# Kernel tuning notes

Measured on AMD Instinct MI355X. Metric: run time of the kernel, lower is better.

The kernel has to match this reference:

```python
import jax, jax.numpy as jnp
import numpy as np

P = 0.8  # DropConnect keep probability
KERNELS = (3, 2)


def eps_contract(core, x, ks):
    """Contract one EPS core with all sliding ks x ks windows of x.
    core: (out, q**(ks*ks)); x: (b, h, w, q) -> (b, h-ks+1, w-ks+1, out).
    Builds the window tensor-product incrementally (small fixed ks*ks loop)."""
    b, h, w, q = x.shape
    H, W = h - ks + 1, w - ks + 1
    prod = None
    for di in range(ks):
        for dj in range(ks):
            pix = x[:, di:di + H, dj:dj + W, :]  # (b, H, W, q)
            if prod is None:
                prod = pix
            else:
                prod = (prod[..., :, None] * pix[..., None, :]).reshape(b, H, W, -1)
    # prod: (b, H, W, q**(ks*ks))
    return jnp.einsum('bhwk,ok->bhwo', prod, core)


def dropconnect_epses(epses):
    """Bernoulli(P) mask each core's components, rescale by 1/P (training mode)."""
    mkey = jax.random.key(42)
    out = []
    for i, core in enumerate(epses):
        mask = (jax.random.uniform(jax.random.fold_in(mkey, i), core.shape) < P).astype(core.dtype)
        out.append(mask * core / P)
    return out


def setup_inputs() -> dict:
    key = jax.random.key(0)
    k0, k1, k2, k3 = jax.random.split(key, 4)
    b = 128
    x = jax.random.uniform(k0, (b, 28, 28, 2), jnp.float32)  # quantum-encoded image
    d0 = 2 ** (3 * 3)   # 512 : first core input dim (q=2, ks=3)
    d1 = 6 ** (2 * 2)   # 1296: second core input dim (q=6, ks=2)
    eps0 = jax.random.normal(k1, (6, d0), jnp.float32) * d0 ** -0.5
    eps1 = jax.random.normal(k2, (10, d1), jnp.float32) * d1 ** -0.5
    in_features = 25 * 25 * 10  # (28 - (3+2) + 2)^2 * out_q
    W = jax.random.normal(k3, (10, in_features), jnp.float32) * (in_features ** -0.5 / 4.0)
    bias = jnp.zeros((10,), jnp.float32)
    return {"x": x, "eps0": eps0, "eps1": eps1, "W": W, "bias": bias}


def reference(x, eps0, eps1, W, bias):
    e0, e1 = dropconnect_epses((eps0, eps1))
    h = eps_contract(e0, x, KERNELS[0])   # (b, 26, 26, 6)
    h = eps_contract(e1, h, KERNELS[1])   # (b, 25, 25, 10)
    flat = h.reshape(h.shape[0], -1)      # b (h w q)
    return flat @ W.T + bias
```

## Files before the change

kernel.cpp:

```cpp
#include <hip/hip_runtime.h>
#include <hip/hip_bf16.h>
#include <stdint.h>

typedef __attribute__((ext_vector_type(8))) short short8;
typedef __attribute__((ext_vector_type(4))) float floatx4;
typedef __attribute__((ext_vector_type(4))) int intx4;

__device__ float h_g[128 * 4056];

__device__ __forceinline__ void threefry2x32(uint32_t k0, uint32_t k1,
                                             uint32_t& x0, uint32_t& x1) {
  const uint32_t ks2 = k0 ^ k1 ^ 0x1BD11BDAu;
  uint32_t ks[3] = {k0, k1, ks2};
  const int rot[8] = {13, 15, 26, 6, 17, 29, 16, 24};
  x0 += ks[0];
  x1 += ks[1];
#pragma unroll
  for (int i = 0; i < 5; ++i) {
#pragma unroll
    for (int j = 0; j < 4; ++j) {
      const int r = rot[(i & 1) * 4 + j];
      x0 += x1;
      x1 = (x1 << r) | (x1 >> (32 - r));
      x1 ^= x0;
    }
    x0 += ks[(i + 1) % 3];
    x1 += ks[(i + 2) % 3] + (uint32_t)(i + 1);
  }
}

struct TFPair { uint32_t x0, x1; };
constexpr TFPair tf_const(uint32_t k0, uint32_t k1, uint32_t x0, uint32_t x1) {
  const uint32_t ks2 = k0 ^ k1 ^ 0x1BD11BDAu;
  uint32_t ks[3] = {k0, k1, ks2};
  const int rot[8] = {13, 15, 26, 6, 17, 29, 16, 24};
  x0 += ks[0];
  x1 += ks[1];
  for (int i = 0; i < 5; ++i) {
    for (int j = 0; j < 4; ++j) {
      const int r = rot[(i & 1) * 4 + j];
      x0 += x1;
      x1 = (x1 << r) | (x1 >> (32 - r));
      x1 ^= x0;
    }
    x0 += ks[(i + 1) % 3];
    x1 += ks[(i + 2) % 3] + (uint32_t)(i + 1);
  }
  return {x0, x1};
}
constexpr TFPair FOLD0 = tf_const(0u, 42u, 0u, 0u);
constexpr TFPair FOLD1 = tf_const(0u, 42u, 0u, 1u);

__device__ __forceinline__ float dropmask(int core, int e, float v) {
  const uint32_t f0 = core ? FOLD1.x0 : FOLD0.x0;
  const uint32_t f1 = core ? FOLD1.x1 : FOLD0.x1;
  uint32_t a = 0u, b = (uint32_t)e;
  threefry2x32(f0, f1, a, b);
  uint32_t bits = a ^ b;
  float u = __uint_as_float((bits >> 9) | 0x3F800000u) - 1.0f;
  float m = (u < 0.8f) ? 1.0f : 0.0f;
  return v * m / 0.8f;
}

__device__ __forceinline__ unsigned short f2bf(float f) {
  uint32_t u = __float_as_uint(f);
  uint32_t r = u + 0x7fffu + ((u >> 16) & 1u);
  return (unsigned short)(r >> 16);
}

union B2I { __hip_bfloat162 b; int i; };
__device__ __forceinline__ int pk_bf16(float lo, float hi) {
  B2I u;
  u.b = __float22bfloat162_rn(make_float2(lo, hi));
  return u.i;
}
union Frag { intx4 i; short8 s; };

__global__ void prep_kernel(const float* __restrict__ eps0,
                            const float* __restrict__ eps1,
                            unsigned short* __restrict__ bsw1,
                            unsigned short* __restrict__ bsw2,
                            const float* __restrict__ bias,
                            float* __restrict__ out) {
  int idx = blockIdx.x * 256 + threadIdx.x;
  if (idx < 1280) out[idx] = bias[idx % 10];
  if (idx < 8192) {
    int j = idx & 7, L = (idx >> 3) & 63, c = idx >> 9;
    int o = L & 15, q = L >> 4;
    int k = c * 32 + q * 8 + j;
    float v = 0.0f;
    if (o < 6) {
      int e = o * 512 + k;
      v = dropmask(0, e, eps0[e]);
    }
    bsw1[idx] = f2bf(v);
  } else {
    int t2 = idx - 8192;
    int j = t2 & 7, L = (t2 >> 3) & 63, c = t2 >> 9;
    int o = L & 15, q = L >> 4;
    int t = 45 * q + c;
    int m = t / 5, nk = 8 * (t % 5) + j;
    float v = 0.0f;
    if (o < 10 && nk < 36) {
      int e = o * 1296 + m * 36 + nk;
      v = dropmask(1, e, eps1[e]);
    }
    bsw2[t2] = f2bf(v);
  }
}

__device__ __forceinline__ float sel6(const float a[6], int k) {
  float r = a[0];
  r = (k == 1) ? a[1] : r;
  r = (k == 2) ? a[2] : r;
  r = (k == 3) ? a[3] : r;
  r = (k == 4) ? a[4] : r;
  r = (k == 5) ? a[5] : r;
  return r;
}

__global__ __launch_bounds__(256, 4) void stage1_kernel(
    const float* __restrict__ x, const unsigned short* __restrict__ bsw1) {
  const int b = blockIdx.y;
  const int t1 = blockIdx.x * 4 + (threadIdx.x >> 6);
  if (t1 >= 43) return;
  const int lane = threadIdx.x & 63;
  const int col = lane & 15, q = lane >> 4;

  intx4 bfr1[16];
  const intx4* bsrc1 = (const intx4*)bsw1;
#pragma unroll
  for (int c = 0; c < 16; ++c) bfr1[c] = bsrc1[c * 64 + lane];

  const float2* x2 = (const float2*)x + b * 784;
  const int p_raw = t1 * 16 + col;
  const int p = p_raw < 676 ? p_raw : 675;
  const int ii = p / 26, jj = p - (p / 26) * 26;

  float xv[9][2];
#pragma unroll
  for (int di = 0; di < 3; ++di)
#pragma unroll
    for (int dj = 0; dj < 3; ++dj) {
      float2 v = x2[(ii + di) * 28 + (jj + dj)];
      xv[di * 3 + dj][0] = v.x;
      xv[di * 3 + dj][1] = v.y;
    }

  float w3[8];
#pragma unroll
  for (int j = 0; j < 8; ++j)
    w3[j] = xv[6][(j >> 2) & 1] * xv[7][(j >> 1) & 1] * xv[8][j & 1];

  const float wq = xv[4][(q >> 1) & 1] * xv[5][q & 1];
  float t01[4], t23[4];
#pragma unroll
  for (int a = 0; a < 2; ++a)
#pragma unroll
    for (int d = 0; d < 2; ++d) {
      t01[a * 2 + d] = xv[0][a] * xv[1][d];
      t23[a * 2 + d] = xv[2][a] * xv[3][d] * wq;
    }

  floatx4 acc0 = {0.f, 0.f, 0.f, 0.f};
  floatx4 acc1 = {0.f, 0.f, 0.f, 0.f};
#pragma unroll
  for (int c = 0; c < 16; ++c) {
    Frag bf;
    bf.i = bfr1[c];
    const float w = t01[c >> 2] * t23[c & 3];
    Frag af;
    af.i.x = pk_bf16(w * w3[0], w * w3[1]);
    af.i.y = pk_bf16(w * w3[2], w * w3[3]);
    af.i.z = pk_bf16(w * w3[4], w * w3[5]);
    af.i.w = pk_bf16(w * w3[6], w * w3[7]);
    if (c & 1)
      acc1 = __builtin_amdgcn_mfma_f32_16x16x32_bf16(af.s, bf.s, acc1, 0, 0, 0);
    else
      acc0 = __builtin_amdgcn_mfma_f32_16x16x32_bf16(af.s, bf.s, acc0, 0, 0, 0);
  }
  const floatx4 acc = acc0 + acc1;
  if (col < 6) {
#pragma unroll
    for (int r = 0; r < 4; ++r) {
      const int pp = t1 * 16 + q * 4 + r;
      if (pp < 676) h_g[b * 4056 + pp * 6 + col] = acc[r];
    }
  }
}

__global__ __launch_bounds__(256, 4) void stage2_kernel(
    const unsigned short* __restrict__ bsw2, const float* __restrict__ W,
    float* __restrict__ out) {
  __shared__ float hs[780];
  __shared__ float flat_t[4][160];

  const int b = blockIdx.y;
  const int tg = blockIdx.x;
  const int tid = threadIdx.x;
  const int wv = tid >> 6;
  const int lane = tid & 63;
  const int col = lane & 15, q = lane >> 4;

  const int r_lo = (tg * 64) / 25;
  const int nrow = (26 - r_lo) < 5 ? (26 - r_lo) : 5;
  const int nflt = nrow * 156;
  for (int i = tid; i < nflt; i += 256) hs[i] = h_g[b * 4056 + r_lo * 156 + i];
  __syncthreads();

  const int tile = tg * 4 + wv;
  const int base2 = tile * 16;
  const int p_raw = base2 + col;
  const int p = p_raw < 625 ? p_raw : 624;
  const int prow = (p * 41) >> 10;
  const int pcol = p - prow * 25;
  const int lr = prow - r_lo;
  const int hbase = (lr * 26 + pcol) * 6;

  float h00[6], h01[6], h10[6], h11[6];
#pragma unroll
  for (int t = 0; t < 6; ++t) {
    h00[t] = hs[hbase + t];
    h01[t] = hs[hbase + 6 + t];
    h10[t] = hs[hbase + 156 + t];
    h11[t] = hs[hbase + 162 + t];
  }

  const intx4* bsrc2 = (const intx4*)bsw2;
  floatx4 acc0 = {0.f, 0.f, 0.f, 0.f};
  floatx4 acc1 = {0.f, 0.f, 0.f, 0.f};
#pragma unroll
  for (int d = 0; d < 9; ++d) {
    const int m = 9 * q + d;
    const int ia = (m * 43) >> 8;
    const int ic = m - ia * 6;
    const float p01 = sel6(h00, ia) * sel6(h01, ic);
    float ph[6];
#pragma unroll
    for (int a = 0; a < 6; ++a) ph[a] = p01 * h10[a];
#pragma unroll
    for (int e = 0; e < 5; ++e) {
      Frag bf;
      bf.i = bsrc2[(d * 5 + e) * 64 + lane];
      const int n0 = 8 * e;
      float av[8];
#pragma unroll
      for (int j = 0; j < 8; ++j) {
        const int n = n0 + j;
        av[j] = (n < 36) ? ph[n / 6] * h11[n % 6] : 0.0f;
      }
      Frag af;
      af.i.x = pk_bf16(av[0], av[1]);
      af.i.y = pk_bf16(av[2], av[3]);
      af.i.z = pk_bf16(av[4], av[5]);
      af.i.w = pk_bf16(av[6], av[7]);
      if (e & 1)
        acc1 = __builtin_amdgcn_mfma_f32_16x16x32_bf16(af.s, bf.s, acc1, 0, 0, 0);
      else
        acc0 = __builtin_amdgcn_mfma_f32_16x16x32_bf16(af.s, bf.s, acc0, 0, 0, 0);
    }
  }
  const floatx4 acc = acc0 + acc1;

  if (col < 10) {
#pragma unroll
    for (int r = 0; r < 4; ++r) {
      const int lp = q * 4 + r;
      flat_t[wv][lp * 10 + col] = (base2 + lp < 625) ? acc[r] : 0.0f;
    }
  }

  float a10[10];
#pragma unroll
  for (int o = 0; o < 10; ++o) a10[o] = 0.0f;
#pragma unroll
  for (int fi = 0; fi < 3; ++fi) {
    const int f = fi * 64 + lane;
    if (f < 160) {
      const float v = flat_t[wv][f];
      int gf = base2 * 10 + f;
      gf = gf < 6250 ? gf : 6249;
#pragma unroll
      for (int o = 0; o < 10; ++o) a10[o] += v * W[o * 6250 + gf];
    }
  }
#pragma unroll
  for (int o = 0; o < 10; ++o) {
#pragma unroll
    for (int s = 32; s > 0; s >>= 1) a10[o] += __shfl_xor(a10[o], s, 64);
  }
  float myv = a10[0];
#pragma unroll
  for (int o = 1; o < 10; ++o) myv = (lane == o) ? a10[o] : myv;
  if (lane < 10) atomicAdd(&out[b * 10 + lane], myv);
}

extern "C" void kernel_launch(void* const* d_in, const int* in_sizes, int n_in,
                              void* d_out, int out_size, void* d_ws,
                              size_t ws_size, hipStream_t stream) {
  const float* x = (const float*)d_in[0];
  const float* eps0 = (const float*)d_in[1];
  const float* eps1 = (const float*)d_in[2];
  const float* W = (const float*)d_in[3];
  const float* bias = (const float*)d_in[4];
  float* out = (float*)d_out;

  char* wsb = (char*)d_ws;
  unsigned short* bsw1 = (unsigned short*)wsb;
  unsigned short* bsw2 = (unsigned short*)(wsb + 16384);

  hipLaunchKernelGGL(prep_kernel, dim3(122), dim3(256), 0, stream, eps0, eps1,
                     bsw1, bsw2, bias, out);
  hipLaunchKernelGGL(stage1_kernel, dim3(11, 128), dim3(256), 0, stream, x,
                     bsw1);
  hipLaunchKernelGGL(stage2_kernel, dim3(10, 128), dim3(256), 0, stream, bsw2,
                     W, out);
}
```

Measured before the change: 99.04 us.

## Process two tiles per wave in both stages to amortize fragment loads

Stage 1 now loops over two 16-pixel tiles per wave, so the preloaded B fragments in registers serve twice the work. Stage 2 handles two tiles per wave, interleaving their MFMAs so each B fragment load from global memory is shared, and stages seven rows of h into shared memory instead of five. Grid sizes are halved and launch bounds lowered to 3 waves per SIMD to allow more registers. The trade-off is fewer blocks and lower occupancy, which could leave the GPU underfilled with only 640 to 768 blocks.

```diff
diff --git a/kernel.cpp b/kernel.cpp
--- a/kernel.cpp
+++ b/kernel.cpp
@@ -119,11 +119,11 @@
   return r;
 }
 
-__global__ __launch_bounds__(256, 4) void stage1_kernel(
+__global__ __launch_bounds__(256, 3) void stage1_kernel(
     const float* __restrict__ x, const unsigned short* __restrict__ bsw1) {
   const int b = blockIdx.y;
-  const int t1 = blockIdx.x * 4 + (threadIdx.x >> 6);
-  if (t1 >= 43) return;
+  const int wv_id = blockIdx.x * 4 + (threadIdx.x >> 6);
+  if (wv_id * 2 >= 43) return;
   const int lane = threadIdx.x & 63;
   const int col = lane & 15, q = lane >> 4;
 
@@ -133,66 +133,73 @@
   for (int c = 0; c < 16; ++c) bfr1[c] = bsrc1[c * 64 + lane];
 
   const float2* x2 = (const float2*)x + b * 784;
-  const int p_raw = t1 * 16 + col;
-  const int p = p_raw < 676 ? p_raw : 675;
-  const int ii = p / 26, jj = p - (p / 26) * 26;
-
-  float xv[9][2];
-#pragma unroll
-  for (int di = 0; di < 3; ++di)
-#pragma unroll
-    for (int dj = 0; dj < 3; ++dj) {
-      float2 v = x2[(ii + di) * 28 + (jj + dj)];
-      xv[di * 3 + dj][0] = v.x;
-      xv[di * 3 + dj][1] = v.y;
-    }
-
-  float w3[8];
-#pragma unroll
-  for (int j = 0; j < 8; ++j)
-    w3[j] = xv[6][(j >> 2) & 1] * xv[7][(j >> 1) & 1] * xv[8][j & 1];
-
-  const float wq = xv[4][(q >> 1) & 1] * xv[5][q & 1];
-  float t01[4], t23[4];
-#pragma unroll
-  for (int a = 0; a < 2; ++a)
-#pragma unroll
-    for (int d = 0; d < 2; ++d) {
-      t01[a * 2 + d] = xv[0][a] * xv[1][d];
-      t23[a * 2 + d] = xv[2][a] * xv[3][d] * wq;
-    }
-
-  floatx4 acc0 = {0.f, 0.f, 0.f, 0.f};
-  floatx4 acc1 = {0.f, 0.f, 0.f, 0.f};
-#pragma unroll
-  for (int c = 0; c < 16; ++c) {
-    Frag bf;
-    bf.i = bfr1[c];
-    const float w = t01[c >> 2] * t23[c & 3];
-    Frag af;
-    af.i.x = pk_bf16(w * w3[0], w * w3[1]);
-    af.i.y = pk_bf16(w * w3[2], w * w3[3]);
-    af.i.z = pk_bf16(w * w3[4], w * w3[5]);
-    af.i.w = pk_bf16(w * w3[6], w * w3[7]);
-    if (c & 1)
-      acc1 = __builtin_amdgcn_mfma_f32_16x16x32_bf16(af.s, bf.s, acc1, 0, 0, 0);
-    else
-      acc0 = __builtin_amdgcn_mfma_f32_16x16x32_bf16(af.s, bf.s, acc0, 0, 0, 0);
-  }
-  const floatx4 acc = acc0 + acc1;
-  if (col < 6) {
-#pragma unroll
-    for (int r = 0; r < 4; ++r) {
-      const int pp = t1 * 16 + q * 4 + r;
-      if (pp < 676) h_g[b * 4056 + pp * 6 + col] = acc[r];
-    }
-  }
-}
-
-__global__ __launch_bounds__(256, 4) void stage2_kernel(
+
+#pragma unroll 1
+  for (int sub = 0; sub < 2; ++sub) {
+    const int t1 = wv_id * 2 + sub;
+    if (t1 >= 43) break;
+
+    const int p_raw = t1 * 16 + col;
+    const int p = p_raw < 676 ? p_raw : 675;
+    const int ii = p / 26, jj = p - (p / 26) * 26;
+
+    float xv[9][2];
+#pragma unroll
+    for (int di = 0; di < 3; ++di)
+#pragma unroll
+      for (int dj = 0; dj < 3; ++dj) {
+        float2 v = x2[(ii + di) * 28 + (jj + dj)];
+        xv[di * 3 + dj][0] = v.x;
+        xv[di * 3 + dj][1] = v.y;
+      }
+
+    float w3[8];
+#pragma unroll
+    for (int j = 0; j < 8; ++j)
+      w3[j] = xv[6][(j >> 2) & 1] * xv[7][(j >> 1) & 1] * xv[8][j & 1];
+
+    const float wq = xv[4][(q >> 1) & 1] * xv[5][q & 1];
+    float t01[4], t23[4];
+#pragma unroll
+    for (int a = 0; a < 2; ++a)
+#pragma unroll
+      for (int d = 0; d < 2; ++d) {
+        t01[a * 2 + d] = xv[0][a] * xv[1][d];
+        t23[a * 2 + d] = xv[2][a] * xv[3][d] * wq;
+      }
+
+    floatx4 acc0 = {0.f, 0.f, 0.f, 0.f};
+    floatx4 acc1 = {0.f, 0.f, 0.f, 0.f};
+#pragma unroll
+    for (int c = 0; c < 16; ++c) {
+      Frag bf;
+      bf.i = bfr1[c];
+      const float w = t01[c >> 2] * t23[c & 3];
+      Frag af;
+      af.i.x = pk_bf16(w * w3[0], w * w3[1]);
+      af.i.y = pk_bf16(w * w3[2], w * w3[3]);
+      af.i.z = pk_bf16(w * w3[4], w * w3[5]);
+      af.i.w = pk_bf16(w * w3[6], w * w3[7]);
+      if (c & 1)
+        acc1 = __builtin_amdgcn_mfma_f32_16x16x32_bf16(af.s, bf.s, acc1, 0, 0, 0);
+      else
+        acc0 = __builtin_amdgcn_mfma_f32_16x16x32_bf16(af.s, bf.s, acc0, 0, 0, 0);
+    }
+    const floatx4 acc = acc0 + acc1;
+    if (col < 6) {
+#pragma unroll
+      for (int r = 0; r < 4; ++r) {
+        const int pp = t1 * 16 + q * 4 + r;
+        if (pp < 676) h_g[b * 4056 + pp * 6 + col] = acc[r];
+      }
+    }
+  }
+}
+
+__global__ __launch_bounds__(256, 3) void stage2_kernel(
     const unsigned short* __restrict__ bsw2, const float* __restrict__ W,
     float* __restrict__ out) {
-  __shared__ float hs[780];
+  __shared__ float hs[1092];
   __shared__ float flat_t[4][160];
 
   const int b = blockIdx.y;
@@ -202,97 +209,130 @@
   const int lane = tid & 63;
   const int col = lane & 15, q = lane >> 4;
 
-  const int r_lo = (tg * 64) / 25;
-  const int nrow = (26 - r_lo) < 5 ? (26 - r_lo) : 5;
+  const int r_lo = (tg * 128) / 25;
+  const int nrow = (26 - r_lo) < 7 ? (26 - r_lo) : 7;
   const int nflt = nrow * 156;
   for (int i = tid; i < nflt; i += 256) hs[i] = h_g[b * 4056 + r_lo * 156 + i];
   __syncthreads();
 
-  const int tile = tg * 4 + wv;
-  const int base2 = tile * 16;
-  const int p_raw = base2 + col;
-  const int p = p_raw < 625 ? p_raw : 624;
-  const int prow = (p * 41) >> 10;
-  const int pcol = p - prow * 25;
-  const int lr = prow - r_lo;
-  const int hbase = (lr * 26 + pcol) * 6;
-
-  float h00[6], h01[6], h10[6], h11[6];
-#pragma unroll
-  for (int t = 0; t < 6; ++t) {
-    h00[t] = hs[hbase + t];
-    h01[t] = hs[hbase + 6 + t];
-    h10[t] = hs[hbase + 156 + t];
-    h11[t] = hs[hbase + 162 + t];
-  }
-
+  const int tileA = tg * 8 + 2 * wv;
   const intx4* bsrc2 = (const intx4*)bsw2;
-  floatx4 acc0 = {0.f, 0.f, 0.f, 0.f};
-  floatx4 acc1 = {0.f, 0.f, 0.f, 0.f};
+
+  float hA[4][6], hB[4][6];
+  int baseT[2];
+#pragma unroll
+  for (int t2i = 0; t2i < 2; ++t2i) {
+    const int base2 = (tileA + t2i) * 16;
+    baseT[t2i] = base2;
+    const int p_raw = base2 + col;
+    const int p = p_raw < 625 ? p_raw : 624;
+    const int prow = (p * 41) >> 10;
+    const int pcol = p - prow * 25;
+    const int lr = prow - r_lo;
+    const int hbase = (lr * 26 + pcol) * 6;
+#pragma unroll
+    for (int t = 0; t < 6; ++t) {
+      float* dst = t2i ? hB[0] : hA[0];
+      dst[0 * 6 + t] = hs[hbase + t];
+      dst[1 * 6 + t] = hs[hbase + 6 + t];
+      dst[2 * 6 + t] = hs[hbase + 156 + t];
+      dst[3 * 6 + t] = hs[hbase + 162 + t];
+    }
+  }
+
+  floatx4 accA0 = {0.f, 0.f, 0.f, 0.f}, accA1 = {0.f, 0.f, 0.f, 0.f};
+  floatx4 accB0 = {0.f, 0.f, 0.f, 0.f}, accB1 = {0.f, 0.f, 0.f, 0.f};
 #pragma unroll
   for (int d = 0; d < 9; ++d) {
     const int m = 9 * q + d;
     const int ia = (m * 43) >> 8;
     const int ic = m - ia * 6;
-    const float p01 = sel6(h00, ia) * sel6(h01, ic);
-    float ph[6];
-#pragma unroll
-    for (int a = 0; a < 6; ++a) ph[a] = p01 * h10[a];
+    const float p01A = sel6(&hA[0][0], ia) * sel6(&hA[1][0], ic);
+    const float p01B = sel6(&hB[0][0], ia) * sel6(&hB[1][0], ic);
+    float phA[6], phB[6];
+#pragma unroll
+    for (int a = 0; a < 6; ++a) {
+      phA[a] = p01A * hA[2][a];
+      phB[a] = p01B * hB[2][a];
+    }
 #pragma unroll
     for (int e = 0; e < 5; ++e) {
       Frag bf;
       bf.i = bsrc2[(d * 5 + e) * 64 + lane];
       const int n0 = 8 * e;
-      float av[8];
-#pragma unroll
-      for (int j = 0; j < 8; ++j) {
-        const int n = n0 + j;
-        av[j] = (n < 36) ? ph[n / 6] * h11[n % 6] : 0.0f;
-      }
-      Frag af;
-      af.i.x = pk_bf16(av[0], av[1]);
-      af.i.y = pk_bf16(av[2], av[3]);
-      af.i.z = pk_bf16(av[4], av[5]);
-      af.i.w = pk_bf16(av[6], av[7]);
-      if (e & 1)
-        acc1 = __builtin_amdgcn_mfma_f32_16x16x32_bf16(af.s, bf.s, acc1, 0, 0, 0);
-      else
-        acc0 = __builtin_amdgcn_mfma_f32_16x16x32_bf16(af.s, bf.s, acc0, 0, 0, 0);
-    }
-  }
-  const floatx4 acc = acc0 + acc1;
-
-  if (col < 10) {
-#pragma unroll
-    for (int r = 0; r < 4; ++r) {
-      const int lp = q * 4 + r;
-      flat_t[wv][lp * 10 + col] = (base2 + lp < 625) ? acc[r] : 0.0f;
-    }
-  }
-
-  float a10[10];
-#pragma unroll
-  for (int o = 0; o < 10; ++o) a10[o] = 0.0f;
-#pragma unroll
-  for (int fi = 0; fi < 3; ++fi) {
-    const int f = fi * 64 + lane;
-    if (f < 160) {
-      const float v = flat_t[wv][f];
-      int gf = base2 * 10 + f;
-      gf = gf < 6250 ? gf : 6249;
-#pragma unroll
-      for (int o = 0; o < 10; ++o) a10[o] += v * W[o * 6250 + gf];
-    }
-  }
-#pragma unroll
-  for (int o = 0; o < 10; ++o) {
-#pragma unroll
-    for (int s = 32; s > 0; s >>= 1) a10[o] += __shfl_xor(a10[o], s, 64);
-  }
-  float myv = a10[0];
-#pragma unroll
-  for (int o = 1; o < 10; ++o) myv = (lane == o) ? a10[o] : myv;
-  if (lane < 10) atomicAdd(&out[b * 10 + lane], myv);
+      {
+        float av[8];
+#pragma unroll
+        for (int j = 0; j < 8; ++j) {
+          const int n = n0 + j;
+          av[j] = (n < 36) ? phA[n / 6] * hA[3][n % 6] : 0.0f;
+        }
+        Frag af;
+        af.i.x = pk_bf16(av[0], av[1]);
+        af.i.y = pk_bf16(av[2], av[3]);
+        af.i.z = pk_bf16(av[4], av[5]);
+        af.i.w = pk_bf16(av[6], av[7]);
+        if (e & 1)
+          accA1 = __builtin_amdgcn_mfma_f32_16x16x32_bf16(af.s, bf.s, accA1, 0, 0, 0);
+        else
+          accA0 = __builtin_amdgcn_mfma_f32_16x16x32_bf16(af.s, bf.s, accA0, 0, 0, 0);
+      }
+      {
+        float av[8];
+#pragma unroll
+        for (int j = 0; j < 8; ++j) {
+          const int n = n0 + j;
+          av[j] = (n < 36) ? phB[n / 6] * hB[3][n % 6] : 0.0f;
+        }
+        Frag af;
+        af.i.x = pk_bf16(av[0], av[1]);
+        af.i.y = pk_bf16(av[2], av[3]);
+        af.i.z = pk_bf16(av[4], av[5]);
+        af.i.w = pk_bf16(av[6], av[7]);
+        if (e & 1)
+          accB1 = __builtin_amdgcn_mfma_f32_16x16x32_bf16(af.s, bf.s, accB1, 0, 0, 0);
+        else
+          accB0 = __builtin_amdgcn_mfma_f32_16x16x32_bf16(af.s, bf.s, accB0, 0, 0, 0);
+      }
+    }
+  }
+
+#pragma unroll 1
+  for (int t2i = 0; t2i < 2; ++t2i) {
+    const int base2 = baseT[t2i];
+    const floatx4 acc = t2i ? (accB0 + accB1) : (accA0 + accA1);
+    if (col < 10) {
+#pragma unroll
+      for (int r = 0; r < 4; ++r) {
+        const int lp = q * 4 + r;
+        flat_t[wv][lp * 10 + col] = (base2 + lp < 625) ? acc[r] : 0.0f;
+      }
+    }
+
+    float a10[10];
+#pragma unroll
+    for (int o = 0; o < 10; ++o) a10[o] = 0.0f;
+#pragma unroll
+    for (int fi = 0; fi < 3; ++fi) {
+      const int f = fi * 64 + lane;
+      if (f < 160) {
+        const float v = flat_t[wv][f];
+        int gf = base2 * 10 + f;
+        gf = gf < 6250 ? gf : 6249;
+#pragma unroll
+        for (int o = 0; o < 10; ++o) a10[o] += v * W[o * 6250 + gf];
+      }
+    }
+#pragma unroll
+    for (int o = 0; o < 10; ++o) {
+#pragma unroll
+      for (int s = 32; s > 0; s >>= 1) a10[o] += __shfl_xor(a10[o], s, 64);
+    }
+    float myv = a10[0];
+#pragma unroll
+    for (int o = 1; o < 10; ++o) myv = (lane == o) ? a10[o] : myv;
+    if (lane < 10) atomicAdd(&out[b * 10 + lane], myv);
+  }
 }
 
 extern "C" void kernel_launch(void* const* d_in, const int* in_sizes, int n_in,
@@ -311,8 +351,8 @@
 
   hipLaunchKernelGGL(prep_kernel, dim3(122), dim3(256), 0, stream, eps0, eps1,
                      bsw1, bsw2, bias, out);
-  hipLaunchKernelGGL(stage1_kernel, dim3(11, 128), dim3(256), 0, stream, x,
+  hipLaunchKernelGGL(stage1_kernel, dim3(6, 128), dim3(256), 0, stream, x,
                      bsw1);
-  hipLaunchKernelGGL(stage2_kernel, dim3(10, 128), dim3(256), 0, stream, bsw2,
+  hipLaunchKernelGGL(stage2_kernel, dim3(5, 128), dim3(256), 0, stream, bsw2,
                      W, out);
 }
```

After: 117.8 us. +19.0%, slower.
